# Optimization experiments

Hardware: AMD Instinct MI355X
Metric: run time of the kernel (lower is better)

The kernel has to match this reference:

```python
import jax, jax.numpy as jnp
import numpy as np

S, T, SP = 4096, 64, 48          # spatial, temporal, seqPredict
P = T - SP                        # predictLength = 16
INP, EMB_H, EMB = 3, 64, 128      # input size, embedding hidden, embedding size
HID, OUT = 256, 128               # LSTM hidden, outputLayer size
FC1, FC2, LG = 256, 64, 32        # output FCNet dims, laneGate hidden


def setup_inputs() -> dict:
    key = jax.random.key(0)
    ks = jax.random.split(key, 32)
    def w(k, shape, fan_in):
        return jax.random.normal(k, shape, dtype=jnp.float32) / np.sqrt(fan_in)
    inp = {}
    inp["inputData"] = jax.random.normal(ks[0], (S, T, INP), dtype=jnp.float32)
    inp["lane"] = jax.random.uniform(ks[1], (S, 1), dtype=jnp.float32)
    # laneGate FCNet: 1 -> LG -> 1
    inp["lgW1"] = w(ks[2], (LG, 1), 1); inp["lgb1"] = jnp.zeros((LG,), jnp.float32)
    inp["lgW2"] = w(ks[3], (1, LG), LG); inp["lgb2"] = jnp.zeros((1,), jnp.float32)
    # embedding FCNet: INP -> EMB_H -> EMB
    inp["eW1"] = w(ks[4], (EMB_H, INP), INP); inp["eb1"] = jnp.zeros((EMB_H,), jnp.float32)
    inp["eW2"] = w(ks[5], (EMB, EMB_H), EMB_H); inp["eb2"] = jnp.zeros((EMB,), jnp.float32)
    # LSTMCell (gate order i, f, g, o)
    inp["Wih"] = w(ks[6], (4 * HID, EMB), EMB)
    inp["Whh"] = w(ks[7], (4 * HID, HID), HID)
    inp["bih"] = jnp.zeros((4 * HID,), jnp.float32)
    inp["bhh"] = jnp.zeros((4 * HID,), jnp.float32)
    # Conv1d(1,1,3,padding=1)
    inp["convw"] = w(ks[8], (3,), 3)
    inp["convb"] = jnp.zeros((1,), jnp.float32)
    # outputLayer: HID -> OUT
    inp["oW"] = w(ks[9], (OUT, HID), HID); inp["ob"] = jnp.zeros((OUT,), jnp.float32)
    # outputs FCNet (addLayer): OUT -> FC1 -> FC2 -> 1
    inp["fW1"] = w(ks[10], (FC1, OUT), OUT); inp["fb1"] = jnp.zeros((FC1,), jnp.float32)
    inp["fW2"] = w(ks[11], (FC2, FC1), FC1); inp["fb2"] = jnp.zeros((FC2,), jnp.float32)
    inp["fW3"] = w(ks[12], (1, FC2), FC2); inp["fb3"] = jnp.zeros((1,), jnp.float32)
    return inp


def reference(inputData, lane, lgW1, lgb1, lgW2, lgb2, eW1, eb1, eW2, eb2,
              Wih, Whh, bih, bhh, convw, convb, oW, ob,
              fW1, fb1, fW2, fb2, fW3, fb3):
    # laneGate: FCNet(1->LG->1) then sigmoid
    lg = jax.nn.relu(lane @ lgW1.T + lgb1) @ lgW2.T + lgb2
    laneC = jax.nn.sigmoid(lg)                       # [S, 1]
    x = inputData * laneC[:, :, None]                # [S, T, INP]
    # embedding FCNet + outer relu
    emb = jax.nn.relu(jax.nn.relu(x @ eW1.T + eb1) @ eW2.T + eb2)  # [S, T, EMB]
    xs = jnp.transpose(emb, (1, 0, 2))               # [T, S, EMB]

    def convpool(h):
        hp = jnp.pad(h, ((0, 0), (1, 1)))
        return convw[0] * hp[:, :-2] + convw[1] * hp[:, 1:-1] + convw[2] * hp[:, 2:] + convb[0]

    def step(carry, x_t):
        h, c = carry
        g = x_t @ Wih.T + bih + h @ Whh.T + bhh      # [S, 4*HID]
        i, f, gg, o = jnp.split(g, 4, axis=-1)
        c = jax.nn.sigmoid(f) * c + jax.nn.sigmoid(i) * jnp.tanh(gg)
        h = jax.nn.sigmoid(o) * jnp.tanh(c)
        h = convpool(h)
        return (h, c), (h, c)

    h0 = jnp.zeros((S, HID), jnp.float32)
    c0 = jnp.zeros((S, HID), jnp.float32)
    # loop 1: time 0 .. SP inclusive (SP+1 steps)
    (h1, c1), (Hs1, Cs1) = jax.lax.scan(step, (h0, c0), xs[:SP + 1])
    # loop 2: time SP .. T-1 (re-processes step SP, overwriting H[:,:,SP])
    (_, _), (Hs2, Cs2) = jax.lax.scan(step, (h1, c1), xs[SP:])

    H = jnp.transpose(jnp.concatenate([Hs1[:SP], Hs2], axis=0), (1, 2, 0))  # [S, HID, T]
    C = jnp.transpose(jnp.concatenate([Cs1[:SP], Cs2], axis=0), (1, 2, 0))

    predict_h = jnp.transpose(Hs2, (1, 0, 2)).reshape(S * P, HID)
    out = predict_h @ oW.T + ob                      # [S*P, OUT]
    out = jax.nn.relu(out @ fW1.T + fb1)
    out = jax.nn.relu(out @ fW2.T + fb2)
    out = out @ fW3.T + fb3                          # [S*P, 1]
    output = out.reshape(S, P) / laneC               # [S, P]
    return (output, H, C)
```

## Files before the change

kernel.cpp:

```cpp
#include <hip/hip_runtime.h>
#include <hip/hip_bf16.h>
#include <stdint.h>

using f32x4  = __attribute__((ext_vector_type(4))) float;
using bf16x8 = __attribute__((ext_vector_type(8))) __bf16;
using short8 = __attribute__((ext_vector_type(8))) short;

__device__ __forceinline__ short f2b(float f) {
    unsigned u = __builtin_bit_cast(unsigned, f);
    unsigned r = (u + 0x7fff + ((u >> 16) & 1)) >> 16;
    return (short)r;
}
__device__ __forceinline__ float b2f(short s) {
    unsigned u = ((unsigned)(unsigned short)s) << 16;
    return __builtin_bit_cast(float, u);
}
__device__ __forceinline__ float sigf(float x) { return 1.f / (1.f + __expf(-x)); }
__device__ __forceinline__ float tanhf_fast(float x) {
    x = fminf(fmaxf(x, -15.f), 15.f);
    float e = __expf(2.f * x);
    return (e - 1.f) / (e + 1.f);
}

__global__ __launch_bounds__(256) void lanec_k(const float* lane, const float* W1, const float* b1,
                                               const float* W2, const float* b2, float* laneC) {
    int s = blockIdx.x * 256 + threadIdx.x;
    float v = lane[s];
    float acc = b2[0];
    #pragma unroll
    for (int k = 0; k < 32; ++k) {
        float t = fmaxf(v * W1[k] + b1[k], 0.f);
        acc += t * W2[k];
    }
    laneC[s] = 1.f / (1.f + __expf(-acc));
}

__global__ __launch_bounds__(256) void pack_k(const float* Wih, const float* Whh, const float* bih,
                                              const float* bhh, const float* oW, const float* fW1,
                                              const float* fW2, const float* eW2,
                                              short* Wcomb, float* biasComb,
                                              short* oWp, short* fW1p, short* fW2p, short* eW2p) {
    int i = blockIdx.x * 256 + threadIdx.x;
    if (i < 393216) {
        int n = i / 384, k = i % 384;
        Wcomb[i] = f2b(k < 128 ? Wih[n * 128 + k] : Whh[n * 256 + (k - 128)]);
        return;
    }
    i -= 393216;
    if (i < 1024) { biasComb[i] = bih[i] + bhh[i]; return; }
    i -= 1024;
    if (i < 32768) { oWp[i] = f2b(oW[i]); return; }
    i -= 32768;
    if (i < 32768) { fW1p[i] = f2b(fW1[i]); return; }
    i -= 32768;
    if (i < 32768) {
        int n = i / 256;
        fW2p[i] = (n < 64) ? f2b(fW2[i]) : (short)0;
        return;
    }
    i -= 32768;
    if (i < 8192) { eW2p[i] = f2b(eW2[i]); return; }
}

__global__ __launch_bounds__(256) void embed1_k(const float* inp, const float* laneC,
                                                const float* eW1, const float* eb1, short* h1) {
    int g = threadIdx.x >> 6, j = threadIdx.x & 63;
    int t = blockIdx.x >> 10;
    int s = ((blockIdx.x & 1023) << 2) + g;
    float lc = laneC[s];
    size_t rin = ((size_t)s * 64 + t) * 3;
    float x0 = inp[rin] * lc, x1 = inp[rin + 1] * lc, x2 = inp[rin + 2] * lc;
    float h = fmaxf(eW1[j * 3] * x0 + eW1[j * 3 + 1] * x1 + eW1[j * 3 + 2] * x2 + eb1[j], 0.f);
    h1[((size_t)t * 4096 + s) * 64 + j] = f2b(h);
}

__global__ __launch_bounds__(256) void init_k(float* cws, short* hb) {
    int i = blockIdx.x * 256 + threadIdx.x;
    cws[i] = 0.f;
    hb[i] = 0;
}

__global__ __launch_bounds__(256) void gemm_k(const short* A1, int K1, const short* A2, int K2,
                                              const short* B, int Kt, const float* bias,
                                              float* outF, short* outB, int Nstore, int Nreal,
                                              int relu) {
    __shared__ alignas(16) short As[128 * 32];
    __shared__ alignas(16) short Bs[128 * 32];
    int tid = threadIdx.x;
    int wave = tid >> 6, lane = tid & 63;
    int m0 = blockIdx.x * 128, n0 = blockIdx.y * 128;

    f32x4 acc[4][4];
    #pragma unroll
    for (int i = 0; i < 4; ++i)
        #pragma unroll
        for (int j = 0; j < 4; ++j) acc[i][j] = (f32x4){0.f, 0.f, 0.f, 0.f};

    const int lr = lane & 15, lk8 = (lane >> 4) * 8;
    const int am = (wave & 1) * 64, bn = (wave >> 1) * 64;
    const int row = tid >> 2, c8 = (tid & 3) * 8;
    int nK = Kt / 32;

    for (int kt = 0; kt < nK; ++kt) {
        int kk = kt * 32;
        const short* Asrc; int astr, acol;
        if (kk < K1) { Asrc = A1; astr = K1; acol = kk; }
        else         { Asrc = A2; astr = K2; acol = kk - K1; }
        short8 a0 = *(const short8*)(Asrc + (size_t)(m0 + row) * astr + acol + c8);
        short8 a1 = *(const short8*)(Asrc + (size_t)(m0 + 64 + row) * astr + acol + c8);
        short8 b0 = *(const short8*)(B + (size_t)(n0 + row) * Kt + kk + c8);
        short8 b1 = *(const short8*)(B + (size_t)(n0 + 64 + row) * Kt + kk + c8);
        __syncthreads();
        *(short8*)&As[tid * 8] = a0;
        *(short8*)&As[(tid + 256) * 8] = a1;
        *(short8*)&Bs[tid * 8] = b0;
        *(short8*)&Bs[(tid + 256) * 8] = b1;
        __syncthreads();
        bf16x8 af[4], bfr[4];
        #pragma unroll
        for (int i = 0; i < 4; ++i) af[i]  = *(const bf16x8*)&As[(am + i * 16 + lr) * 32 + lk8];
        #pragma unroll
        for (int j = 0; j < 4; ++j) bfr[j] = *(const bf16x8*)&Bs[(bn + j * 16 + lr) * 32 + lk8];
        #pragma unroll
        for (int i = 0; i < 4; ++i)
            #pragma unroll
            for (int j = 0; j < 4; ++j)
                acc[i][j] = __builtin_amdgcn_mfma_f32_16x16x32_bf16(af[i], bfr[j], acc[i][j], 0, 0, 0);
    }

    int r0 = m0 + am + (lane >> 4) * 4;
    int c0 = n0 + bn + (lane & 15);
    #pragma unroll
    for (int j = 0; j < 4; ++j) {
        int col = c0 + j * 16;
        if (col >= Nreal) continue;
        float bs = bias[col];
        #pragma unroll
        for (int i = 0; i < 4; ++i) {
            #pragma unroll
            for (int r = 0; r < 4; ++r) {
                int rw = r0 + i * 16 + r;
                float v = acc[i][j][r] + bs;
                if (relu) v = fmaxf(v, 0.f);
                size_t o = (size_t)rw * Nstore + col;
                if (outF) outF[o] = v;
                if (outB) outB[o] = f2b(v);
            }
        }
    }
}

__global__ __launch_bounds__(256) void pointwise_k(const float* gates, float* cws, short* hb,
                                                   const float* convw, const float* convb,
                                                   float* Hdst, float* Cdst, short* predictb,
                                                   int tslot, int doWrite, int staged, int pslot) {
    __shared__ float sh[258];
    int s = blockIdx.x, j = threadIdx.x;
    size_t gbase = (size_t)s * 1024 + j;
    float gi = gates[gbase], gf = gates[gbase + 256], gg = gates[gbase + 512], go = gates[gbase + 768];
    size_t cidx = (size_t)s * 256 + j;
    float c = cws[cidx];
    c = sigf(gf) * c + sigf(gi) * tanhf_fast(gg);
    float hraw = sigf(go) * tanhf_fast(c);
    if (j == 0) { sh[0] = 0.f; sh[257] = 0.f; }
    sh[j + 1] = hraw;
    __syncthreads();
    float h = convw[0] * sh[j] + convw[1] * sh[j + 1] + convw[2] * sh[j + 2] + convb[0];
    cws[cidx] = c;
    hb[cidx] = f2b(h);
    if (doWrite) {
        size_t oidx = staged ? (((size_t)s * 64 + tslot) * 256 + j)
                             : (((size_t)s * 256 + j) * 64 + tslot);
        Hdst[oidx] = h;
        Cdst[oidx] = c;
    }
    if (pslot >= 0) predictb[((size_t)s * 16 + pslot) * 256 + j] = f2b(h);
}

__global__ __launch_bounds__(256) void transpose_k(const float* Hs, const float* Cs,
                                                   float* Ho, float* Co) {
    __shared__ float tile[64][129];
    int s = blockIdx.x, jh = blockIdx.y;
    const float* src = blockIdx.z ? Cs : Hs;
    float* dst = blockIdx.z ? Co : Ho;
    #pragma unroll 4
    for (int i = 0; i < 32; ++i) {
        int idx = i * 256 + threadIdx.x;
        int t = idx >> 7, jj = idx & 127;
        tile[t][jj] = src[((size_t)s * 64 + t) * 256 + jh * 128 + jj];
    }
    __syncthreads();
    #pragma unroll 4
    for (int i = 0; i < 32; ++i) {
        int idx = i * 256 + threadIdx.x;
        int jj = idx >> 6, t = idx & 63;
        dst[((size_t)s * 256 + jh * 128 + jj) * 64 + t] = tile[t][jj];
    }
}

__global__ __launch_bounds__(256) void final_k(const short* t2b, const float* fW3, const float* fb3,
                                               const float* laneC, float* out0) {
    int r = blockIdx.x * 256 + threadIdx.x;
    float acc = fb3[0];
    const short* rowp = t2b + (size_t)r * 64;
    #pragma unroll 8
    for (int k = 0; k < 64; ++k) acc += b2f(rowp[k]) * fW3[k];
    out0[r] = acc / laneC[r >> 4];
}

extern "C" void kernel_launch(void* const* d_in, const int* in_sizes, int n_in,
                              void* d_out, int out_size, void* d_ws, size_t ws_size,
                              hipStream_t stream) {
    (void)in_sizes; (void)n_in; (void)out_size;
    const float* inputData = (const float*)d_in[0];
    const float* lane  = (const float*)d_in[1];
    const float* lgW1  = (const float*)d_in[2];  const float* lgb1 = (const float*)d_in[3];
    const float* lgW2  = (const float*)d_in[4];  const float* lgb2 = (const float*)d_in[5];
    const float* eW1   = (const float*)d_in[6];  const float* eb1  = (const float*)d_in[7];
    const float* eW2   = (const float*)d_in[8];  const float* eb2  = (const float*)d_in[9];
    const float* Wih   = (const float*)d_in[10]; const float* Whh  = (const float*)d_in[11];
    const float* bih   = (const float*)d_in[12]; const float* bhh  = (const float*)d_in[13];
    const float* convw = (const float*)d_in[14]; const float* convb= (const float*)d_in[15];
    const float* oW    = (const float*)d_in[16]; const float* ob   = (const float*)d_in[17];
    const float* fW1   = (const float*)d_in[18]; const float* fb1  = (const float*)d_in[19];
    const float* fW2   = (const float*)d_in[20]; const float* fb2  = (const float*)d_in[21];
    const float* fW3   = (const float*)d_in[22]; const float* fb3  = (const float*)d_in[23];

    float* out0 = (float*)d_out;
    float* Hout = out0 + 65536;
    float* Cout = Hout + (size_t)67108864;

    char* w = (char*)d_ws;
    size_t off = 0;
    auto alloc = [&](size_t bytes) -> void* {
        void* p = w + off;
        off += (bytes + 255) & ~(size_t)255;
        return p;
    };
    float* laneC    = (float*)alloc(4096 * 4);
    float* biasComb = (float*)alloc(1024 * 4);
    short* Wcomb    = (short*)alloc((size_t)1024 * 384 * 2);
    short* oWp      = (short*)alloc((size_t)128 * 256 * 2);
    short* fW1p     = (short*)alloc((size_t)256 * 128 * 2);
    short* fW2p     = (short*)alloc((size_t)128 * 256 * 2);
    short* eW2p     = (short*)alloc((size_t)128 * 64 * 2);
    short* h1       = (short*)alloc((size_t)64 * 4096 * 64 * 2);
    short* xs       = (short*)alloc((size_t)64 * 4096 * 128 * 2);
    short* hb       = (short*)alloc((size_t)4096 * 256 * 2);
    float* cws      = (float*)alloc((size_t)4096 * 256 * 4);
    float* gates    = (float*)alloc((size_t)4096 * 1024 * 4);
    short* predictb = (short*)alloc((size_t)65536 * 256 * 2);
    short* t0b      = (short*)alloc((size_t)65536 * 128 * 2);
    short* t1b      = (short*)alloc((size_t)65536 * 256 * 2);
    short* t2b      = (short*)alloc((size_t)65536 * 64 * 2);
    float* Hstage   = (float*)alloc((size_t)4096 * 64 * 256 * 4);
    float* Cstage   = (float*)alloc((size_t)4096 * 64 * 256 * 4);
    bool staged = ws_size >= off;

    lanec_k<<<16, 256, 0, stream>>>(lane, lgW1, lgb1, lgW2, lgb2, laneC);
    {
        int total = 393216 + 1024 + 32768 + 32768 + 32768 + 8192;
        pack_k<<<(total + 255) / 256, 256, 0, stream>>>(Wih, Whh, bih, bhh, oW, fW1, fW2, eW2,
                                                        Wcomb, biasComb, oWp, fW1p, fW2p, eW2p);
    }
    embed1_k<<<65536, 256, 0, stream>>>(inputData, laneC, eW1, eb1, h1);
    gemm_k<<<dim3(2048, 1), 256, 0, stream>>>(h1, 64, (const short*)nullptr, 0, eW2p, 64,
                                              eb2, (float*)nullptr, xs, 128, 128, 1);
    init_k<<<4096, 256, 0, stream>>>(cws, hb);

    for (int k = 0; k < 65; ++k) {
        int it = (k <= 48) ? k : k - 1;
        gemm_k<<<dim3(32, 8), 256, 0, stream>>>(xs + (size_t)it * 4096 * 128, 128, hb, 256,
                                                Wcomb, 384, biasComb, gates, (short*)nullptr,
                                                1024, 1024, 0);
        int tslot = (k < 48) ? k : k - 1;
        int doW = (k == 48) ? 0 : 1;
        int pslot = (k >= 49) ? (k - 49) : -1;
        float* Hd = staged ? Hstage : Hout;
        float* Cd = staged ? Cstage : Cout;
        pointwise_k<<<4096, 256, 0, stream>>>(gates, cws, hb, convw, convb, Hd, Cd, predictb,
                                              tslot, doW, staged ? 1 : 0, pslot);
    }
    if (staged)
        transpose_k<<<dim3(4096, 2, 2), 256, 0, stream>>>(Hstage, Cstage, Hout, Cout);

    gemm_k<<<dim3(512, 1), 256, 0, stream>>>(predictb, 256, (const short*)nullptr, 0, oWp, 256,
                                             ob, (float*)nullptr, t0b, 128, 128, 0);
    gemm_k<<<dim3(512, 2), 256, 0, stream>>>(t0b, 128, (const short*)nullptr, 0, fW1p, 128,
                                             fb1, (float*)nullptr, t1b, 256, 256, 1);
    gemm_k<<<dim3(512, 1), 256, 0, stream>>>(t1b, 256, (const short*)nullptr, 0, fW2p, 256,
                                             fb2, (float*)nullptr, t2b, 64, 64, 1);
    final_k<<<256, 256, 0, stream>>>(t2b, fW3, fb3, laneC, out0);
}
```

Baseline: 2.100 ms.

## Fuse LSTM recurrence into one persistent kernel with register-resident weights

Replaces the 65 per-timestep GEMM and pointwise launch pairs with a single persistent kernel. Each 1024-thread block owns 16 sequences, keeps the full combined Wih/Whh weight slice in registers as bf16 MFMA operands, and keeps h in LDS and c in registers across all 65 steps. The gate rows are permuted at pack time so each wave computes i/f/g/o for the same hidden units, which lets the cell update run directly on the MFMA accumulators with no global gates buffer. Sigmoid and tanh now use a hardware reciprocal. In exchange there are only 256 blocks, very high register pressure from 48 weight vectors per thread, and a serial dependency chain inside each block.

```diff
diff --git a/kernel.cpp b/kernel.cpp
--- a/kernel.cpp
+++ b/kernel.cpp
@@ -15,11 +15,12 @@
     unsigned u = ((unsigned)(unsigned short)s) << 16;
     return __builtin_bit_cast(float, u);
 }
-__device__ __forceinline__ float sigf(float x) { return 1.f / (1.f + __expf(-x)); }
+__device__ __forceinline__ float sigf(float x) {
+    return __builtin_amdgcn_rcpf(1.f + __expf(-x));
+}
 __device__ __forceinline__ float tanhf_fast(float x) {
     x = fminf(fmaxf(x, -15.f), 15.f);
-    float e = __expf(2.f * x);
-    return (e - 1.f) / (e + 1.f);
+    return 2.f * __builtin_amdgcn_rcpf(1.f + __expf(-2.f * x)) - 1.f;
 }
 
 __global__ __launch_bounds__(256) void lanec_k(const float* lane, const float* W1, const float* b1,
@@ -38,16 +39,26 @@
 __global__ __launch_bounds__(256) void pack_k(const float* Wih, const float* Whh, const float* bih,
                                               const float* bhh, const float* oW, const float* fW1,
                                               const float* fW2, const float* eW2,
-                                              short* Wcomb, float* biasComb,
+                                              short* pW, float* biasP,
                                               short* oWp, short* fW1p, short* fW2p, short* eW2p) {
     int i = blockIdx.x * 256 + threadIdx.x;
     if (i < 393216) {
-        int n = i / 384, k = i % 384;
-        Wcomb[i] = f2b(k < 128 ? Wih[n * 128 + k] : Whh[n * 256 + (k - 128)]);
+        int p = i / 384, k = i % 384;
+        int g = (p >> 4) & 3;
+        int j = ((p >> 6) << 4) | (p & 15);
+        int n = g * 256 + j;
+        pW[i] = f2b(k < 128 ? Wih[n * 128 + k] : Whh[n * 256 + (k - 128)]);
         return;
     }
     i -= 393216;
-    if (i < 1024) { biasComb[i] = bih[i] + bhh[i]; return; }
+    if (i < 1024) {
+        int p = i;
+        int g = (p >> 4) & 3;
+        int j = ((p >> 6) << 4) | (p & 15);
+        int n = g * 256 + j;
+        biasP[p] = bih[n] + bhh[n];
+        return;
+    }
     i -= 1024;
     if (i < 32768) { oWp[i] = f2b(oW[i]); return; }
     i -= 32768;
@@ -72,12 +83,6 @@
     float x0 = inp[rin] * lc, x1 = inp[rin + 1] * lc, x2 = inp[rin + 2] * lc;
     float h = fmaxf(eW1[j * 3] * x0 + eW1[j * 3 + 1] * x1 + eW1[j * 3 + 2] * x2 + eb1[j], 0.f);
     h1[((size_t)t * 4096 + s) * 64 + j] = f2b(h);
-}
-
-__global__ __launch_bounds__(256) void init_k(float* cws, short* hb) {
-    int i = blockIdx.x * 256 + threadIdx.x;
-    cws[i] = 0.f;
-    hb[i] = 0;
 }
 
 __global__ __launch_bounds__(256) void gemm_k(const short* A1, int K1, const short* A2, int K2,
@@ -150,31 +155,79 @@
     }
 }
 
-__global__ __launch_bounds__(256) void pointwise_k(const float* gates, float* cws, short* hb,
-                                                   const float* convw, const float* convb,
-                                                   float* Hdst, float* Cdst, short* predictb,
-                                                   int tslot, int doWrite, int staged, int pslot) {
-    __shared__ float sh[258];
-    int s = blockIdx.x, j = threadIdx.x;
-    size_t gbase = (size_t)s * 1024 + j;
-    float gi = gates[gbase], gf = gates[gbase + 256], gg = gates[gbase + 512], go = gates[gbase + 768];
-    size_t cidx = (size_t)s * 256 + j;
-    float c = cws[cidx];
-    c = sigf(gf) * c + sigf(gi) * tanhf_fast(gg);
-    float hraw = sigf(go) * tanhf_fast(c);
-    if (j == 0) { sh[0] = 0.f; sh[257] = 0.f; }
-    sh[j + 1] = hraw;
-    __syncthreads();
-    float h = convw[0] * sh[j] + convw[1] * sh[j + 1] + convw[2] * sh[j + 2] + convb[0];
-    cws[cidx] = c;
-    hb[cidx] = f2b(h);
-    if (doWrite) {
-        size_t oidx = staged ? (((size_t)s * 64 + tslot) * 256 + j)
-                             : (((size_t)s * 256 + j) * 64 + tslot);
-        Hdst[oidx] = h;
-        Cdst[oidx] = c;
-    }
-    if (pslot >= 0) predictb[((size_t)s * 16 + pslot) * 256 + j] = f2b(h);
+__global__ __launch_bounds__(1024) void lstm_k(const short* xs, const short* pW, const float* biasP,
+                                               const float* convw, const float* convb,
+                                               float* Hd, float* Cd, short* predictb, int staged) {
+    __shared__ alignas(16) short A[16][392];
+    __shared__ float hraw[16][258];
+
+    const int tid = threadIdx.x;
+    const int w = tid >> 6, l = tid & 63;
+    const int lj = l & 15, lk = l >> 4;
+    const int j = (w << 4) | lj;
+    const int s4 = lk * 4;
+    const int s0 = blockIdx.x * 16;
+
+    bf16x8 wreg[4][12];
+    #pragma unroll
+    for (int g = 0; g < 4; ++g)
+        #pragma unroll
+        for (int kk = 0; kk < 12; ++kk)
+            wreg[g][kk] = *(const bf16x8*)(pW + ((size_t)(64 * w + 16 * g + lj)) * 384 + kk * 32 + lk * 8);
+    float bias_g[4];
+    #pragma unroll
+    for (int g = 0; g < 4; ++g) bias_g[g] = biasP[64 * w + 16 * g + lj];
+    float creg[4] = {0.f, 0.f, 0.f, 0.f};
+    const float cw0 = convw[0], cw1 = convw[1], cw2 = convw[2], cb = convb[0];
+
+    for (int i = tid; i < 16 * 256; i += 1024) A[i >> 8][128 + (i & 255)] = 0;
+    if (tid < 16) { hraw[tid][0] = 0.f; hraw[tid][257] = 0.f; }
+
+    for (int k = 0; k < 65; ++k) {
+        int it = (k <= 48) ? k : k - 1;
+        {
+            int r = tid >> 6, c2 = (tid & 63) * 2;
+            *(int*)&A[r][c2] = *(const int*)(xs + ((size_t)it * 4096 + s0 + r) * 128 + c2);
+        }
+        __syncthreads();
+
+        f32x4 acc[4];
+        #pragma unroll
+        for (int g = 0; g < 4; ++g) acc[g] = (f32x4){bias_g[g], bias_g[g], bias_g[g], bias_g[g]};
+        #pragma unroll
+        for (int kk = 0; kk < 12; ++kk) {
+            bf16x8 af = *(const bf16x8*)&A[lj][kk * 32 + lk * 8];
+            #pragma unroll
+            for (int g = 0; g < 4; ++g)
+                acc[g] = __builtin_amdgcn_mfma_f32_16x16x32_bf16(af, wreg[g][kk], acc[g], 0, 0, 0);
+        }
+
+        #pragma unroll
+        for (int r = 0; r < 4; ++r) {
+            float gi = acc[0][r], gf = acc[1][r], gg = acc[2][r], go = acc[3][r];
+            float c = sigf(gf) * creg[r] + sigf(gi) * tanhf_fast(gg);
+            creg[r] = c;
+            hraw[s4 + r][j + 1] = sigf(go) * tanhf_fast(c);
+        }
+        __syncthreads();
+
+        int tslot = (k < 48) ? k : k - 1;
+        int doW = (k != 48);
+        int pslot = k - 49;
+        #pragma unroll
+        for (int r = 0; r < 4; ++r) {
+            int s = s4 + r;
+            float h = cw0 * hraw[s][j] + cw1 * hraw[s][j + 1] + cw2 * hraw[s][j + 2] + cb;
+            A[s][128 + j] = f2b(h);
+            if (doW) {
+                size_t o = staged ? (((size_t)(s0 + s) * 64 + tslot) * 256 + j)
+                                  : (((size_t)(s0 + s) * 256 + j) * 64 + tslot);
+                Hd[o] = h;
+                Cd[o] = creg[r];
+            }
+            if (pslot >= 0) predictb[((size_t)(s0 + s) * 16 + pslot) * 256 + j] = f2b(h);
+        }
+    }
 }
 
 __global__ __launch_bounds__(256) void transpose_k(const float* Hs, const float* Cs,
@@ -238,17 +291,14 @@
         return p;
     };
     float* laneC    = (float*)alloc(4096 * 4);
-    float* biasComb = (float*)alloc(1024 * 4);
-    short* Wcomb    = (short*)alloc((size_t)1024 * 384 * 2);
+    float* biasP    = (float*)alloc(1024 * 4);
+    short* pW       = (short*)alloc((size_t)1024 * 384 * 2);
     short* oWp      = (short*)alloc((size_t)128 * 256 * 2);
     short* fW1p     = (short*)alloc((size_t)256 * 128 * 2);
     short* fW2p     = (short*)alloc((size_t)128 * 256 * 2);
     short* eW2p     = (short*)alloc((size_t)128 * 64 * 2);
     short* h1       = (short*)alloc((size_t)64 * 4096 * 64 * 2);
     short* xs       = (short*)alloc((size_t)64 * 4096 * 128 * 2);
-    short* hb       = (short*)alloc((size_t)4096 * 256 * 2);
-    float* cws      = (float*)alloc((size_t)4096 * 256 * 4);
-    float* gates    = (float*)alloc((size_t)4096 * 1024 * 4);
     short* predictb = (short*)alloc((size_t)65536 * 256 * 2);
     short* t0b      = (short*)alloc((size_t)65536 * 128 * 2);
     short* t1b      = (short*)alloc((size_t)65536 * 256 * 2);
@@ -261,26 +311,16 @@
     {
         int total = 393216 + 1024 + 32768 + 32768 + 32768 + 8192;
         pack_k<<<(total + 255) / 256, 256, 0, stream>>>(Wih, Whh, bih, bhh, oW, fW1, fW2, eW2,
-                                                        Wcomb, biasComb, oWp, fW1p, fW2p, eW2p);
+                                                        pW, biasP, oWp, fW1p, fW2p, eW2p);
     }
     embed1_k<<<65536, 256, 0, stream>>>(inputData, laneC, eW1, eb1, h1);
     gemm_k<<<dim3(2048, 1), 256, 0, stream>>>(h1, 64, (const short*)nullptr, 0, eW2p, 64,
                                               eb2, (float*)nullptr, xs, 128, 128, 1);
-    init_k<<<4096, 256, 0, stream>>>(cws, hb);
-
-    for (int k = 0; k < 65; ++k) {
-        int it = (k <= 48) ? k : k - 1;
-        gemm_k<<<dim3(32, 8), 256, 0, stream>>>(xs + (size_t)it * 4096 * 128, 128, hb, 256,
-                                                Wcomb, 384, biasComb, gates, (short*)nullptr,
-                                                1024, 1024, 0);
-        int tslot = (k < 48) ? k : k - 1;
-        int doW = (k == 48) ? 0 : 1;
-        int pslot = (k >= 49) ? (k - 49) : -1;
-        float* Hd = staged ? Hstage : Hout;
-        float* Cd = staged ? Cstage : Cout;
-        pointwise_k<<<4096, 256, 0, stream>>>(gates, cws, hb, convw, convb, Hd, Cd, predictb,
-                                              tslot, doW, staged ? 1 : 0, pslot);
-    }
+
+    float* Hd = staged ? Hstage : Hout;
+    float* Cd = staged ? Cstage : Cout;
+    lstm_k<<<256, 1024, 0, stream>>>(xs, pW, biasP, convw, convb, Hd, Cd, predictb,
+                                     staged ? 1 : 0);
     if (staged)
         transpose_k<<<dim3(4096, 2, 2), 256, 0, stream>>>(Hstage, Cstage, Hout, Cout);
 
```

New measurement: 1.725 ms. 17.9% less time.
